# Optimization experiments

Hardware: AMD Instinct MI355X
Metric: run time of the kernel (lower is better)

## Reference

```python
import jax, jax.numpy as jnp
import numpy as np

D_MODEL = 512
N = 2048
BS = 8


def setup_inputs() -> dict:
    key = jax.random.key(0)
    ks = jax.random.split(key, 5)
    inputs1 = jax.random.normal(ks[0], (BS, N, D_MODEL), dtype=jnp.float32)
    inputs2 = jax.random.normal(ks[1], (BS, N, D_MODEL), dtype=jnp.float32)
    # torch Linear weights: init.normal_(std=0.001), bias=0
    Wq = 0.001 * jax.random.normal(ks[2], (D_MODEL, D_MODEL), dtype=jnp.float32)
    Wk = 0.001 * jax.random.normal(ks[3], (D_MODEL, D_MODEL), dtype=jnp.float32)
    Wv = 0.001 * jax.random.normal(ks[4], (D_MODEL, D_MODEL), dtype=jnp.float32)
    bq = jnp.zeros((D_MODEL,), dtype=jnp.float32)
    bk = jnp.zeros((D_MODEL,), dtype=jnp.float32)
    bv = jnp.zeros((D_MODEL,), dtype=jnp.float32)
    # nn.Parameter(torch.ones((n, n)))
    position_biases = jnp.ones((N, N), dtype=jnp.float32)
    return {"inputs1": inputs1, "inputs2": inputs2, "Wq": Wq, "bq": bq,
            "Wk": Wk, "bk": bk, "Wv": Wv, "bv": bv,
            "position_biases": position_biases}


def reference(inputs1, inputs2, Wq, bq, Wk, bk, Wv, bv, position_biases):
    # torch Linear: y = x @ W.T + b
    q = inputs1 @ Wq.T + bq                     # [b, n, d]
    k = inputs1 @ Wk.T + bk                     # [b, s, d]
    v = inputs2 @ Wv.T + bv                     # [b, s, d]
    # exp(k[b,s,d] + bias[t,s]) = exp(bias)[t,s] * exp(k)[b,s,d] -> separable,
    # avoiding the original's (n, bs, n, dim) broadcast intermediate.
    expB = jnp.exp(position_biases)             # [t, s]
    ek = jnp.exp(k)                             # [b, s, d]
    num = jnp.einsum('ts,bsd->btd', expB, ek * v)
    den = jnp.einsum('ts,bsd->btd', expB, ek)
    return jax.nn.sigmoid(q) * (num / den)      # [b, n, d]
```

## Files before the change

### kernel.cpp

```cpp
#include <hip/hip_runtime.h>

typedef float  f32x4  __attribute__((ext_vector_type(4)));
typedef __bf16 bf16x8 __attribute__((ext_vector_type(8)));
typedef __bf16 bf16x4 __attribute__((ext_vector_type(4)));

#define D_MODEL 512
#define SEQ     2048
#define BATCH   8
#define ROWS    (BATCH * SEQ)

#define ASYNC_COPY16(dst_lds, src_glb)                                          \
  __builtin_amdgcn_global_load_lds(                                             \
      (const __attribute__((address_space(1))) void*)(src_glb),                 \
      (__attribute__((address_space(3))) void*)(dst_lds), 16, 0, 0)

__global__ void cvt_all_kernel(const float* __restrict__ x1,
                               const float* __restrict__ x2,
                               const float* __restrict__ posb,
                               const float* __restrict__ Wq,
                               const float* __restrict__ Wk,
                               const float* __restrict__ Wv,
                               __bf16* __restrict__ x1b, __bf16* __restrict__ x2b,
                               __bf16* __restrict__ expBb, __bf16* __restrict__ wb)
{
  const int blk = blockIdx.x;
  if (blk < 16384) {
    const float* in = (blk < 8192) ? x1 : x2;
    __bf16* out = (blk < 8192) ? x1b : x2b;
    const int i = (blk & 8191) * 256 + threadIdx.x;
    float4 v = ((const float4*)in)[i];
    bf16x4 o = { (__bf16)v.x, (__bf16)v.y, (__bf16)v.z, (__bf16)v.w };
    ((bf16x4*)out)[i] = o;
  } else if (blk < 20480) {
    const int i = (blk - 16384) * 256 + threadIdx.x;
    float4 v = ((const float4*)posb)[i];
    bf16x4 o = { (__bf16)__expf(v.x), (__bf16)__expf(v.y),
                 (__bf16)__expf(v.z), (__bf16)__expf(v.w) };
    ((bf16x4*)expBb)[i] = o;
  } else {
    const int i = (blk - 20480) * 256 + threadIdx.x;
    const int nW4 = D_MODEL * D_MODEL / 4;
    const float* src = (i < nW4) ? Wq : (i < 2 * nW4) ? Wk : Wv;
    const int ii = i - ((i < nW4) ? 0 : (i < 2 * nW4) ? nW4 : 2 * nW4);
    float4 v = ((const float4*)src)[ii];
    bf16x4 o = { (__bf16)v.x, (__bf16)v.y, (__bf16)v.z, (__bf16)v.w };
    ((bf16x4*)wb)[i] = o;
  }
}

__global__ __launch_bounds__(256) void tri_gemm_kernel(
    const __bf16* __restrict__ x1b, const __bf16* __restrict__ x2b,
    const __bf16* __restrict__ wb,
    const float* __restrict__ bq, const float* __restrict__ bk,
    const float* __restrict__ bv,
    __bf16* __restrict__ sigq, __bf16* __restrict__ kT,
    __bf16* __restrict__ vT)
{
  __shared__ __align__(16) __bf16 As[2][128 * 64];
  __shared__ __align__(16) __bf16 Bs[2][128 * 64];

  const int K = D_MODEL;
  const int z = blockIdx.z;
  const int tid  = threadIdx.x;
  const int wave = tid >> 6;
  const int lane = tid & 63;
  const int quad = lane >> 4;
  const int l16  = lane & 15;
  const int wm   = (wave >> 1) * 64;
  const int wn   = (wave & 1) * 64;
  const int l8r = lane >> 3;
  const int scol = ((lane & 7) ^ l8r) * 8;
  const int F0 = blockIdx.y * 128;

  const __bf16* Ap = (z == 0) ? x1b
                   : (z == 1) ? (wb + (long long)D_MODEL * D_MODEL)
                              : (wb + 2LL * D_MODEL * D_MODEL);
  const __bf16* Bp = (z == 0) ? wb : (z == 1) ? x1b : x2b;

  const int srow = wave * 8 + l8r;

  const __bf16* ga[4]; const __bf16* gb[4];
  auto set_tile = [&](int t) {
    const int L0 = (blockIdx.x * 2 + t) * 128;
    const int m0 = (z == 0) ? L0 : F0;
    const int n0 = (z == 0) ? F0 : L0;
    #pragma unroll
    for (int i = 0; i < 4; ++i) {
      ga[i] = Ap + (long long)(m0 + i * 32 + srow) * K + scol;
      gb[i] = Bp + (long long)(n0 + i * 32 + srow) * K + scol;
    }
  };
  auto stageA = [&](int c, int k0) {
    #pragma unroll
    for (int i = 0; i < 4; ++i)
      ASYNC_COPY16(&As[c][(i * 32 + wave * 8) * 64], ga[i] + k0);
  };
  auto stageB = [&](int c, int k0) {
    #pragma unroll
    for (int i = 0; i < 4; ++i)
      ASYNC_COPY16(&Bs[c][(i * 32 + wave * 8) * 64], gb[i] + k0);
  };

  set_tile(0);
  stageA(0, 0);
  stageB(0, 0);

  f32x4 acc[4][4];
  #pragma unroll
  for (int i = 0; i < 4; ++i)
    #pragma unroll
    for (int j = 0; j < 4; ++j) acc[i][j] = (f32x4){0.f, 0.f, 0.f, 0.f};

  for (int s = 0; s < 16; ++s) {
    const int c = s & 1;
    asm volatile("s_waitcnt vmcnt(0)" ::: "memory");
    __builtin_amdgcn_s_barrier();
    __builtin_amdgcn_sched_barrier(0);

    const bool pf = (s + 1 < 16);
    const int k1 = ((s + 1) & 7) * 64;

    #pragma unroll
    for (int kk = 0; kk < 2; ++kk) {
      const int slot = ((quad + kk * 4) ^ (l16 & 7)) * 8;
      bf16x8 af[4], bfr[4];
      #pragma unroll
      for (int i = 0; i < 4; ++i)
        af[i] = *(const bf16x8*)&As[c][(wm + i * 16 + l16) * 64 + slot];
      #pragma unroll
      for (int j = 0; j < 4; ++j)
        bfr[j] = *(const bf16x8*)&Bs[c][(wn + j * 16 + l16) * 64 + slot];
      if (pf) {
        if (kk == 0) {
          if (s == 7) set_tile(1);
          stageA(c ^ 1, k1);
        } else {
          stageB(c ^ 1, k1);
        }
      }
      __builtin_amdgcn_s_barrier();
      asm volatile("s_waitcnt lgkmcnt(0)" ::: "memory");
      __builtin_amdgcn_sched_barrier(0);
      __builtin_amdgcn_s_setprio(1);
      #pragma unroll
      for (int i = 0; i < 4; ++i)
        #pragma unroll
        for (int j = 0; j < 4; ++j)
          acc[i][j] = __builtin_amdgcn_mfma_f32_16x16x32_bf16(af[i], bfr[j],
                                                              acc[i][j], 0, 0, 0);
      __builtin_amdgcn_s_setprio(0);
      __builtin_amdgcn_s_barrier();
    }

    if ((s & 7) == 7) {
      const int t = s >> 3;
      const int L0 = (blockIdx.x * 2 + t) * 128;
      if (z == 0) {
        const int m0 = L0, n0 = F0;
        #pragma unroll
        for (int j = 0; j < 4; ++j) {
          const int col = n0 + wn + j * 16 + l16;
          const float bvv = bq[col];
          #pragma unroll
          for (int i = 0; i < 4; ++i)
            #pragma unroll
            for (int r = 0; r < 4; ++r) {
              const int row = m0 + wm + i * 16 + quad * 4 + r;
              float x = acc[i][j][r] + bvv;
              sigq[(long long)row * D_MODEL + col] =
                  (__bf16)(1.f / (1.f + __expf(-x)));
            }
        }
      } else {
        const int m0 = F0, n0 = L0;
        const float* bias = (z == 1) ? bk : bv;
        __bf16* outp = (z == 1) ? kT : vT;
        #pragma unroll
        for (int i = 0; i < 4; ++i) {
          #pragma unroll
          for (int r = 0; r < 4; ++r) {
            const int d = m0 + wm + i * 16 + quad * 4 + r;
            const float bvv = bias[d];
            #pragma unroll
            for (int j = 0; j < 4; ++j) {
              const int rr = n0 + wn + j * 16 + l16;
              outp[(long long)d * ROWS + rr] = (__bf16)(acc[i][j][r] + bvv);
            }
          }
        }
      }
      if (s == 7) {
        #pragma unroll
        for (int i = 0; i < 4; ++i)
          #pragma unroll
          for (int j = 0; j < 4; ++j) acc[i][j] = (f32x4){0.f, 0.f, 0.f, 0.f};
      }
    }
  }
}

__global__ __launch_bounds__(256) void combine_kernel(
    const __bf16* __restrict__ kT, const __bf16* __restrict__ vT,
    __bf16* __restrict__ ekvT)
{
  const int c = blockIdx.x * 256 + threadIdx.x;
  const int d   = c >> 11;
  const int off = (c & 2047) * 8;
  const int b = off >> 11;
  const int s = off & 2047;

  bf16x8 kk = *(const bf16x8*)(kT + (long long)d * ROWS + off);
  bf16x8 vv = *(const bf16x8*)(vT + (long long)d * ROWS + off);
  bf16x8 ek, ev;
  #pragma unroll
  for (int e = 0; e < 8; ++e) {
    float ekf = __expf((float)kk[e]);
    ek[e] = (__bf16)ekf;
    ev[e] = (__bf16)(ekf * (float)vv[e]);
  }
  const int gr = ((d >> 5) << 6) + (d & 31);
  __bf16* outp = ekvT + (long long)b * (2 * D_MODEL) * SEQ + s;
  *(bf16x8*)(outp + (long long)gr * SEQ)        = ev;
  *(bf16x8*)(outp + (long long)(gr + 32) * SEQ) = ek;
}

#define EBM 256
#define EBN 256
#define EBK 64
#define ENT (SEQ / EBK)

__global__ __launch_bounds__(512) void einsum_fused_kernel(
    const __bf16* __restrict__ A, const __bf16* __restrict__ BtAll,
    const __bf16* __restrict__ sigq, float* __restrict__ out)
{
  extern __shared__ __align__(16) __bf16 smem[];

  const int b = blockIdx.z;
  const __bf16* Bt = BtAll + (long long)b * (2 * D_MODEL) * SEQ;

  const int tid  = threadIdx.x;
  const int wave = tid >> 6;
  const int lane = tid & 63;
  const int quad = lane >> 4;
  const int l16  = lane & 15;
  const int wm   = (wave >> 2) * 128;
  const int wn   = (wave & 3) * 64;
  const int m0   = blockIdx.x * EBM;
  const int n0   = blockIdx.y * EBN;
  const int l8r  = lane >> 3;
  const int scol = ((lane & 7) ^ l8r) * 8;

  const __bf16* gA = A  + (long long)(m0 + wave * 8 + l8r) * SEQ + scol;
  const __bf16* gB = Bt + (long long)(n0 + wave * 8 + l8r) * SEQ + scol;
  __bf16* lA = smem +         (wave * 8) * 64;
  __bf16* lB = smem + 32768 + (wave * 8) * 64;

  f32x4 acc[8][4];
  #pragma unroll
  for (int i = 0; i < 8; ++i)
    #pragma unroll
    for (int j = 0; j < 4; ++j) acc[i][j] = (f32x4){0.f, 0.f, 0.f, 0.f};

  auto stage_pair = [&](int c, int k0, int i) {
    ASYNC_COPY16(lA + c * 16384 + i * 4096, gA + (long long)i * 64 * SEQ + k0);
    ASYNC_COPY16(lB + c * 16384 + i * 4096, gB + (long long)i * 64 * SEQ + k0);
  };

  #pragma unroll
  for (int i = 0; i < 4; ++i) stage_pair(0, 0, i);

  const int s0 = ((quad    ) ^ (l16 & 7)) * 8;
  const int s1 = ((quad + 4) ^ (l16 & 7)) * 8;

  for (int t = 0; t < ENT; ++t) {
    const int c = t & 1;
    asm volatile("s_waitcnt vmcnt(0)" ::: "memory");
    __builtin_amdgcn_s_barrier();
    __builtin_amdgcn_sched_barrier(0);

    const __bf16* Ac = smem +         c * 16384 + (wm + l16) * 64;
    const __bf16* Bc = smem + 32768 + c * 16384 + (wn + l16) * 64;
    const bool pf = (t + 1 < ENT);
    const int k1 = (t + 1) * EBK;

    bf16x8 bfr[4][2];
    #pragma unroll
    for (int q = 0; q < 4; ++q) {
      if (q == 0) {
        #pragma unroll
        for (int j = 0; j < 4; ++j) {
          bfr[j][0] = *(const bf16x8*)&Bc[j * 1024 + s0];
          bfr[j][1] = *(const bf16x8*)&Bc[j * 1024 + s1];
        }
      }
      bf16x8 af[2][2];
      #pragma unroll
      for (int ii = 0; ii < 2; ++ii) {
        af[ii][0] = *(const bf16x8*)&Ac[(q * 2 + ii) * 1024 + s0];
        af[ii][1] = *(const bf16x8*)&Ac[(q * 2 + ii) * 1024 + s1];
      }
      if (pf) {
        if (q == 0) { stage_pair(c ^ 1, k1, 0); stage_pair(c ^ 1, k1, 1); }
        else if (q == 1) { stage_pair(c ^ 1, k1, 2); stage_pair(c ^ 1, k1, 3); }
      }
      __builtin_amdgcn_s_barrier();
      asm volatile("s_waitcnt lgkmcnt(0)" ::: "memory");
      __builtin_amdgcn_sched_barrier(0);
      __builtin_amdgcn_s_setprio(1);
      #pragma unroll
      for (int kk = 0; kk < 2; ++kk)
        #pragma unroll
        for (int ii = 0; ii < 2; ++ii)
          #pragma unroll
          for (int j = 0; j < 4; ++j)
            acc[q * 2 + ii][j] = __builtin_amdgcn_mfma_f32_16x16x32_bf16(
                af[ii][kk], bfr[j][kk], acc[q * 2 + ii][j], 0, 0, 0);
      __builtin_amdgcn_s_setprio(0);
      __builtin_amdgcn_s_barrier();
    }
  }

  const int g = (n0 + wn) >> 6;
  #pragma unroll
  for (int j = 0; j < 2; ++j) {
    const int d = g * 32 + j * 16 + l16;
    #pragma unroll
    for (int i = 0; i < 8; ++i) {
      #pragma unroll
      for (int r = 0; r < 4; ++r) {
        const int row = m0 + wm + i * 16 + quad * 4 + r;
        const long long off = ((long long)b * SEQ + row) * D_MODEL + d;
        const float num = acc[i][j][r];
        const float den = acc[i][j + 2][r];
        out[off] = (float)sigq[off] * (num / den);
      }
    }
  }
}

extern "C" void kernel_launch(void* const* d_in, const int* in_sizes, int n_in,
                              void* d_out, int out_size, void* d_ws, size_t ws_size,
                              hipStream_t stream) {
  const float* inputs1 = (const float*)d_in[0];
  const float* inputs2 = (const float*)d_in[1];
  const float* Wq = (const float*)d_in[2];
  const float* bq = (const float*)d_in[3];
  const float* Wk = (const float*)d_in[4];
  const float* bk = (const float*)d_in[5];
  const float* Wv = (const float*)d_in[6];
  const float* bv = (const float*)d_in[7];
  const float* posb = (const float*)d_in[8];
  float* out = (float*)d_out;

  char* ws = (char*)d_ws;
  const long long szX  = (long long)ROWS * D_MODEL * 2;
  const long long szW  = (long long)D_MODEL * D_MODEL * 2;
  const long long szEB = (long long)SEQ * SEQ * 2;
  const long long szT  = (long long)BATCH * 2 * D_MODEL * SEQ * 2;
  __bf16* x1b   = (__bf16*)(ws);                 ws += szX;
  __bf16* x2b   = (__bf16*)(ws);                 ws += szX;
  __bf16* wb    = (__bf16*)(ws);                 ws += 3 * szW;
  __bf16* expBb = (__bf16*)(ws);                 ws += szEB;
  __bf16* sigq  = (__bf16*)(ws);                 ws += szX;
  __bf16* kT    = (__bf16*)(ws);                 ws += szX;
  __bf16* vT    = (__bf16*)(ws);                 ws += szX;
  __bf16* ekvT  = (__bf16*)(ws);                 ws += szT;

  static bool attr_done = false;
  if (!attr_done) {
    hipFuncSetAttribute((const void*)einsum_fused_kernel,
                        hipFuncAttributeMaxDynamicSharedMemorySize, 131072);
    attr_done = true;
  }

  cvt_all_kernel<<<21248, 256, 0, stream>>>(inputs1, inputs2, posb,
                                            Wq, Wk, Wv,
                                            x1b, x2b, expBb, wb);

  {
    dim3 g(ROWS / 256, D_MODEL / 128, 3);
    tri_gemm_kernel<<<g, 256, 0, stream>>>(x1b, x2b, wb, bq, bk, bv,
                                           sigq, kT, vT);
  }

  combine_kernel<<<(D_MODEL * ROWS / 8) / 256, 256, 0, stream>>>(kT, vT, ekvT);

  {
    dim3 g(SEQ / EBM, (2 * D_MODEL) / EBN, BATCH);
    einsum_fused_kernel<<<g, 512, 131072, stream>>>(expBb, ekvT, sigq, out);
  }
}
```

Baseline: 275.7 us.

## Enlarge tri-GEMM tile to 256x256 with 512 threads and dynamic LDS

The projection GEMM now uses 256x256 output tiles computed by 8 waves, each holding a 128x64 accumulator, with 128KB of dynamic shared memory. Previously each 256-thread block computed two consecutive 128x128 tiles. The larger tile raises operand reuse and cuts global and LDS traffic per FLOP. In exchange it uses more registers and LDS per block, which lowers occupancy, and the grid shrinks to 384 blocks, which may underfill the GPU.

After: 254.1 us. 7.8% less time.

```diff
diff --git a/kernel.cpp b/kernel.cpp
--- a/kernel.cpp
+++ b/kernel.cpp
@@ -48,7 +48,9 @@
   }
 }
 
-__global__ __launch_bounds__(256) void tri_gemm_kernel(
+#define TNT (D_MODEL / 64)
+
+__global__ __launch_bounds__(512) void tri_gemm_kernel(
     const __bf16* __restrict__ x1b, const __bf16* __restrict__ x2b,
     const __bf16* __restrict__ wb,
     const float* __restrict__ bq, const float* __restrict__ bk,
@@ -56,8 +58,7 @@
     __bf16* __restrict__ sigq, __bf16* __restrict__ kT,
     __bf16* __restrict__ vT)
 {
-  __shared__ __align__(16) __bf16 As[2][128 * 64];
-  __shared__ __align__(16) __bf16 Bs[2][128 * 64];
+  extern __shared__ __align__(16) __bf16 smem[];
 
   const int K = D_MODEL;
   const int z = blockIdx.z;
@@ -66,134 +67,120 @@
   const int lane = tid & 63;
   const int quad = lane >> 4;
   const int l16  = lane & 15;
-  const int wm   = (wave >> 1) * 64;
-  const int wn   = (wave & 1) * 64;
-  const int l8r = lane >> 3;
+  const int wm   = (wave >> 2) * 128;
+  const int wn   = (wave & 3) * 64;
+  const int L0   = blockIdx.x * 256;
+  const int F0   = blockIdx.y * 256;
+  const int m0   = (z == 0) ? L0 : F0;
+  const int n0   = (z == 0) ? F0 : L0;
+  const int l8r  = lane >> 3;
   const int scol = ((lane & 7) ^ l8r) * 8;
-  const int F0 = blockIdx.y * 128;
 
   const __bf16* Ap = (z == 0) ? x1b
                    : (z == 1) ? (wb + (long long)D_MODEL * D_MODEL)
                               : (wb + 2LL * D_MODEL * D_MODEL);
   const __bf16* Bp = (z == 0) ? wb : (z == 1) ? x1b : x2b;
 
-  const int srow = wave * 8 + l8r;
-
-  const __bf16* ga[4]; const __bf16* gb[4];
-  auto set_tile = [&](int t) {
-    const int L0 = (blockIdx.x * 2 + t) * 128;
-    const int m0 = (z == 0) ? L0 : F0;
-    const int n0 = (z == 0) ? F0 : L0;
-    #pragma unroll
-    for (int i = 0; i < 4; ++i) {
-      ga[i] = Ap + (long long)(m0 + i * 32 + srow) * K + scol;
-      gb[i] = Bp + (long long)(n0 + i * 32 + srow) * K + scol;
-    }
+  const __bf16* gA = Ap + (long long)(m0 + wave * 8 + l8r) * K + scol;
+  const __bf16* gB = Bp + (long long)(n0 + wave * 8 + l8r) * K + scol;
+  __bf16* lA = smem +         (wave * 8) * 64;
+  __bf16* lB = smem + 32768 + (wave * 8) * 64;
+
+  f32x4 acc[8][4];
+  #pragma unroll
+  for (int i = 0; i < 8; ++i)
+    #pragma unroll
+    for (int j = 0; j < 4; ++j) acc[i][j] = (f32x4){0.f, 0.f, 0.f, 0.f};
+
+  auto stage_pair = [&](int c, int k0, int i) {
+    ASYNC_COPY16(lA + c * 16384 + i * 4096, gA + (long long)i * 64 * K + k0);
+    ASYNC_COPY16(lB + c * 16384 + i * 4096, gB + (long long)i * 64 * K + k0);
   };
-  auto stageA = [&](int c, int k0) {
-    #pragma unroll
-    for (int i = 0; i < 4; ++i)
-      ASYNC_COPY16(&As[c][(i * 32 + wave * 8) * 64], ga[i] + k0);
-  };
-  auto stageB = [&](int c, int k0) {
-    #pragma unroll
-    for (int i = 0; i < 4; ++i)
-      ASYNC_COPY16(&Bs[c][(i * 32 + wave * 8) * 64], gb[i] + k0);
-  };
-
-  set_tile(0);
-  stageA(0, 0);
-  stageB(0, 0);
-
-  f32x4 acc[4][4];
-  #pragma unroll
-  for (int i = 0; i < 4; ++i)
-    #pragma unroll
-    for (int j = 0; j < 4; ++j) acc[i][j] = (f32x4){0.f, 0.f, 0.f, 0.f};
-
-  for (int s = 0; s < 16; ++s) {
-    const int c = s & 1;
+
+  #pragma unroll
+  for (int i = 0; i < 4; ++i) stage_pair(0, 0, i);
+
+  const int s0 = ((quad    ) ^ (l16 & 7)) * 8;
+  const int s1 = ((quad + 4) ^ (l16 & 7)) * 8;
+
+  for (int t = 0; t < TNT; ++t) {
+    const int c = t & 1;
     asm volatile("s_waitcnt vmcnt(0)" ::: "memory");
     __builtin_amdgcn_s_barrier();
     __builtin_amdgcn_sched_barrier(0);
 
-    const bool pf = (s + 1 < 16);
-    const int k1 = ((s + 1) & 7) * 64;
-
-    #pragma unroll
-    for (int kk = 0; kk < 2; ++kk) {
-      const int slot = ((quad + kk * 4) ^ (l16 & 7)) * 8;
-      bf16x8 af[4], bfr[4];
-      #pragma unroll
-      for (int i = 0; i < 4; ++i)
-        af[i] = *(const bf16x8*)&As[c][(wm + i * 16 + l16) * 64 + slot];
-      #pragma unroll
-      for (int j = 0; j < 4; ++j)
-        bfr[j] = *(const bf16x8*)&Bs[c][(wn + j * 16 + l16) * 64 + slot];
+    const __bf16* Ac = smem +         c * 16384 + (wm + l16) * 64;
+    const __bf16* Bc = smem + 32768 + c * 16384 + (wn + l16) * 64;
+    const bool pf = (t + 1 < TNT);
+    const int k1 = (t + 1) * 64;
+
+    bf16x8 bfr[4][2];
+    #pragma unroll
+    for (int q = 0; q < 4; ++q) {
+      if (q == 0) {
+        #pragma unroll
+        for (int j = 0; j < 4; ++j) {
+          bfr[j][0] = *(const bf16x8*)&Bc[j * 1024 + s0];
+          bfr[j][1] = *(const bf16x8*)&Bc[j * 1024 + s1];
+        }
+      }
+      bf16x8 af[2][2];
+      #pragma unroll
+      for (int ii = 0; ii < 2; ++ii) {
+        af[ii][0] = *(const bf16x8*)&Ac[(q * 2 + ii) * 1024 + s0];
+        af[ii][1] = *(const bf16x8*)&Ac[(q * 2 + ii) * 1024 + s1];
+      }
       if (pf) {
-        if (kk == 0) {
-          if (s == 7) set_tile(1);
-          stageA(c ^ 1, k1);
-        } else {
-          stageB(c ^ 1, k1);
-        }
+        if (q == 0) { stage_pair(c ^ 1, k1, 0); stage_pair(c ^ 1, k1, 1); }
+        else if (q == 1) { stage_pair(c ^ 1, k1, 2); stage_pair(c ^ 1, k1, 3); }
       }
       __builtin_amdgcn_s_barrier();
       asm volatile("s_waitcnt lgkmcnt(0)" ::: "memory");
       __builtin_amdgcn_sched_barrier(0);
       __builtin_amdgcn_s_setprio(1);
       #pragma unroll
-      for (int i = 0; i < 4; ++i)
-        #pragma unroll
-        for (int j = 0; j < 4; ++j)
-          acc[i][j] = __builtin_amdgcn_mfma_f32_16x16x32_bf16(af[i], bfr[j],
-                                                              acc[i][j], 0, 0, 0);
+      for (int kk = 0; kk < 2; ++kk)
+        #pragma unroll
+        for (int ii = 0; ii < 2; ++ii)
+          #pragma unroll
+          for (int j = 0; j < 4; ++j)
+            acc[q * 2 + ii][j] = __builtin_amdgcn_mfma_f32_16x16x32_bf16(
+                af[ii][kk], bfr[j][kk], acc[q * 2 + ii][j], 0, 0, 0);
       __builtin_amdgcn_s_setprio(0);
       __builtin_amdgcn_s_barrier();
     }
-
-    if ((s & 7) == 7) {
-      const int t = s >> 3;
-      const int L0 = (blockIdx.x * 2 + t) * 128;
-      if (z == 0) {
-        const int m0 = L0, n0 = F0;
+  }
+
+  if (z == 0) {
+    #pragma unroll
+    for (int j = 0; j < 4; ++j) {
+      const int col = n0 + wn + j * 16 + l16;
+      const float bvv = bq[col];
+      #pragma unroll
+      for (int i = 0; i < 8; ++i) {
+        #pragma unroll
+        for (int r = 0; r < 4; ++r) {
+          const int row = m0 + wm + i * 16 + quad * 4 + r;
+          float x = acc[i][j][r] + bvv;
+          sigq[(long long)row * D_MODEL + col] =
+              (__bf16)(1.f / (1.f + __expf(-x)));
+        }
+      }
+    }
+  } else {
+    const float* bias = (z == 1) ? bk : bv;
+    __bf16* outp = (z == 1) ? kT : vT;
+    #pragma unroll
+    for (int i = 0; i < 8; ++i) {
+      #pragma unroll
+      for (int r = 0; r < 4; ++r) {
+        const int d = m0 + wm + i * 16 + quad * 4 + r;
+        const float bvv = bias[d];
         #pragma unroll
         for (int j = 0; j < 4; ++j) {
-          const int col = n0 + wn + j * 16 + l16;
-          const float bvv = bq[col];
-          #pragma unroll
-          for (int i = 0; i < 4; ++i)
-            #pragma unroll
-            for (int r = 0; r < 4; ++r) {
-              const int row = m0 + wm + i * 16 + quad * 4 + r;
-              float x = acc[i][j][r] + bvv;
-              sigq[(long long)row * D_MODEL + col] =
-                  (__bf16)(1.f / (1.f + __expf(-x)));
-            }
+          const int rr = n0 + wn + j * 16 + l16;
+          outp[(long long)d * ROWS + rr] = (__bf16)(acc[i][j][r] + bvv);
         }
-      } else {
-        const int m0 = F0, n0 = L0;
-        const float* bias = (z == 1) ? bk : bv;
-        __bf16* outp = (z == 1) ? kT : vT;
-        #pragma unroll
-        for (int i = 0; i < 4; ++i) {
-          #pragma unroll
-          for (int r = 0; r < 4; ++r) {
-            const int d = m0 + wm + i * 16 + quad * 4 + r;
-            const float bvv = bias[d];
-            #pragma unroll
-            for (int j = 0; j < 4; ++j) {
-              const int rr = n0 + wn + j * 16 + l16;
-              outp[(long long)d * ROWS + rr] = (__bf16)(acc[i][j][r] + bvv);
-            }
-          }
-        }
-      }
-      if (s == 7) {
-        #pragma unroll
-        for (int i = 0; i < 4; ++i)
-          #pragma unroll
-          for (int j = 0; j < 4; ++j) acc[i][j] = (f32x4){0.f, 0.f, 0.f, 0.f};
       }
     }
   }
@@ -370,6 +357,8 @@
   if (!attr_done) {
     hipFuncSetAttribute((const void*)einsum_fused_kernel,
                         hipFuncAttributeMaxDynamicSharedMemorySize, 131072);
+    hipFuncSetAttribute((const void*)tri_gemm_kernel,
+                        hipFuncAttributeMaxDynamicSharedMemorySize, 131072);
     attr_done = true;
   }
 
@@ -378,9 +367,9 @@
                                             x1b, x2b, expBb, wb);
 
   {
-    dim3 g(ROWS / 256, D_MODEL / 128, 3);
-    tri_gemm_kernel<<<g, 256, 0, stream>>>(x1b, x2b, wb, bq, bk, bv,
-                                           sigq, kT, vT);
+    dim3 g(ROWS / 256, D_MODEL / 256, 3);
+    tri_gemm_kernel<<<g, 512, 131072, stream>>>(x1b, x2b, wb, bq, bk, bv,
+                                                sigq, kT, vT);
   }
 
   combine_kernel<<<(D_MODEL * ROWS / 8) / 256, 256, 0, stream>>>(kT, vT, ekvT);
```
